# Optimization experiments

Hardware: AMD Instinct MI355X
Metric: run time of the kernel (lower is better)

## Reference

```python
import jax, jax.numpy as jnp
import numpy as np

B, T, D, H = 256, 1024, 64, 128


def _orthogonal(key, shape):
    a = jax.random.normal(key, (max(shape), max(shape)), dtype=jnp.float32)
    q, _ = jnp.linalg.qr(a)
    return q[: shape[0], : shape[1]].astype(jnp.float32)


def setup_inputs() -> dict:
    key = jax.random.key(0)
    k0, k1, k2, k3 = jax.random.split(key, 4)
    x = jax.random.normal(k0, (B, T, D), dtype=jnp.float32)
    W_xK = _orthogonal(k1, (H, D))
    W_xz = _orthogonal(k2, (H, D))
    W_hK = _orthogonal(k3, (H, H))
    b_xK = jnp.zeros((H,), jnp.float32)
    b_xz = jnp.zeros((H,), jnp.float32)
    b_hK = jnp.zeros((H,), jnp.float32)
    return {"x": x, "W_xK": W_xK, "b_xK": b_xK, "W_xz": W_xz,
            "b_xz": b_xz, "W_hK": W_hK, "b_hK": b_hK}


def reference(x, W_xK, b_xK, W_xz, b_xz, W_hK, b_hK):
    # Precompute input projections for all timesteps (batched GEMM).
    gate_x_K = jnp.einsum('btd,hd->bth', x, W_xK) + b_xK  # [B,T,H]
    gate_x_z = jnp.einsum('btd,hd->bth', x, W_xz) + b_xz  # [B,T,H]
    z_all = jnp.tanh(gate_x_z)                             # [B,T,H]
    h0 = jnp.zeros((x.shape[0], W_hK.shape[0]), x.dtype)

    def step(h, inputs):
        gxK, z = inputs  # each [B,H]
        gate_h_K = h @ W_hK.T + b_hK
        K_gain = jax.nn.sigmoid(gxK + gate_h_K)
        h_new = jnp.tanh(h + K_gain * (z - h))
        return h_new, h_new

    # scan over time dim
    _, outs = jax.lax.scan(step, h0,
                           (jnp.swapaxes(gate_x_K, 0, 1),
                            jnp.swapaxes(z_all, 0, 1)))
    outs = jnp.swapaxes(outs, 0, 1)  # [B,T,H]
    return (outs, outs)
```

## Files before the change

### kernel.cpp

```cpp
#include <hip/hip_runtime.h>
#include <hip/hip_fp16.h>

#define NB 256
#define NT 1024
#define ND 64
#define NH 128

typedef __fp16 half8 __attribute__((ext_vector_type(8)));
typedef float float4v __attribute__((ext_vector_type(4)));

static __device__ __forceinline__ float fast_tanh(float v) {
    float e = __expf(2.0f * v);
    return 1.0f - 2.0f * __builtin_amdgcn_rcpf(e + 1.0f);
}

static __device__ __forceinline__ void fast_barrier() {
    asm volatile("s_waitcnt lgkmcnt(0)\n\ts_barrier" ::: "memory");
}

__global__ __launch_bounds__(256, 1) void fused_rnn_mfma(
        const float* __restrict__ x,
        const float* __restrict__ WxK, const float* __restrict__ bxK,
        const float* __restrict__ Wxz, const float* __restrict__ bxz,
        const float* __restrict__ Whk, const float* __restrict__ bhk,
        float* __restrict__ out) {
    __shared__ __align__(16) __fp16 hbuf[2][128];
    __shared__ __align__(16) __fp16 gbuf[2][16][132];
    __shared__ __align__(16) __fp16 zbuf[2][16][132];

    const int tid = threadIdx.x;
    const int b = blockIdx.x;
    const int wid = tid >> 6, lane = tid & 63;
    const int l16 = lane & 15, kg = lane >> 4;
    const int jl = lane & 31;
    const int j = wid * 32 + jl;

    half8 whT[2][4];
    half8 wxT[2][2][2];
    float bGK[2], bZ[2];
    #pragma unroll
    for (int ct = 0; ct < 2; ++ct) {
        const int row = wid * 32 + ct * 16 + l16;
        #pragma unroll
        for (int kt = 0; kt < 4; ++kt) {
            const float* p = Whk + (size_t)row * NH + kt * 32 + kg * 8;
            float4v u = *(const float4v*)p, v = *(const float4v*)(p + 4);
            whT[ct][kt] = (half8){(__fp16)u.x, (__fp16)u.y, (__fp16)u.z, (__fp16)u.w,
                                  (__fp16)v.x, (__fp16)v.y, (__fp16)v.z, (__fp16)v.w};
        }
        #pragma unroll
        for (int mat = 0; mat < 2; ++mat) {
            const float* W = mat ? Wxz : WxK;
            #pragma unroll
            for (int kt = 0; kt < 2; ++kt) {
                const float* p = W + (size_t)row * ND + kt * 32 + kg * 8;
                float4v u = *(const float4v*)p, v = *(const float4v*)(p + 4);
                wxT[mat][ct][kt] = (half8){(__fp16)u.x, (__fp16)u.y, (__fp16)u.z, (__fp16)u.w,
                                           (__fp16)v.x, (__fp16)v.y, (__fp16)v.z, (__fp16)v.w};
            }
        }
        bGK[ct] = bxK[row] + bhk[row];
        bZ[ct]  = bxz[row];
    }
    const float4v zero4 = {0.f, 0.f, 0.f, 0.f};

    const float* xb = x + (size_t)b * NT * ND;
    float4v xf[4];

    auto xload = [&](int c) {
        const float* px = xb + (size_t)c * 16 * 64 + (size_t)l16 * 64;
        #pragma unroll
        for (int kt = 0; kt < 2; ++kt) {
            const float* q = px + kt * 32 + kg * 8;
            xf[2 * kt]     = *(const float4v*)q;
            xf[2 * kt + 1] = *(const float4v*)(q + 4);
        }
    };

    auto proj = [&](int dst) {
        half8 ax[2];
        #pragma unroll
        for (int kt = 0; kt < 2; ++kt) {
            float4v u = xf[2 * kt], v = xf[2 * kt + 1];
            ax[kt] = (half8){(__fp16)u.x, (__fp16)u.y, (__fp16)u.z, (__fp16)u.w,
                             (__fp16)v.x, (__fp16)v.y, (__fp16)v.z, (__fp16)v.w};
        }
        #pragma unroll
        for (int mat = 0; mat < 2; ++mat)
            #pragma unroll
            for (int ct = 0; ct < 2; ++ct) {
                float4v pc = __builtin_amdgcn_mfma_f32_16x16x32_f16(ax[0], wxT[mat][ct][0], zero4, 0, 0, 0);
                pc = __builtin_amdgcn_mfma_f32_16x16x32_f16(ax[1], wxT[mat][ct][1], pc, 0, 0, 0);
                const int col = wid * 32 + ct * 16 + l16;
                #pragma unroll
                for (int r = 0; r < 4; ++r) {
                    const int row = kg * 4 + r;
                    if (mat == 0) gbuf[dst][row][col] = (__fp16)(pc[r] + bGK[ct]);
                    else          zbuf[dst][row][col] = (__fp16)fast_tanh(pc[r] + bZ[ct]);
                }
            }
    };

    xload(0);
    if (tid < 128) hbuf[0][tid] = (__fp16)0.0f;
    proj(0);
    xload(1);
    __syncthreads();

    float hn = 0.0f;
    float oreg[16];
    const size_t CPY = (size_t)NB * NT * NH;
    float* ob = out + (size_t)b * NT * NH + j;

    for (int c = 0; c < 64; ++c) {
        const int cb = c & 1;

        #pragma unroll
        for (int s = 0; s < 16; ++s) {
            const int p = s & 1;
            half8 ah0 = *(const half8*)&hbuf[p][0 * 32 + kg * 8];
            half8 ah1 = *(const half8*)&hbuf[p][1 * 32 + kg * 8];
            half8 ah2 = *(const half8*)&hbuf[p][2 * 32 + kg * 8];
            half8 ah3 = *(const half8*)&hbuf[p][3 * 32 + kg * 8];
            const float gv = (float)gbuf[cb][s][j];
            const float zv = (float)zbuf[cb][s][j];

            float4v aA0 = __builtin_amdgcn_mfma_f32_16x16x32_f16(ah0, whT[0][0], zero4, 0, 0, 0);
            float4v aA1 = __builtin_amdgcn_mfma_f32_16x16x32_f16(ah0, whT[1][0], zero4, 0, 0, 0);
            float4v aB0 = __builtin_amdgcn_mfma_f32_16x16x32_f16(ah2, whT[0][2], zero4, 0, 0, 0);
            float4v aB1 = __builtin_amdgcn_mfma_f32_16x16x32_f16(ah2, whT[1][2], zero4, 0, 0, 0);
            aA0 = __builtin_amdgcn_mfma_f32_16x16x32_f16(ah1, whT[0][1], aA0, 0, 0, 0);
            aA1 = __builtin_amdgcn_mfma_f32_16x16x32_f16(ah1, whT[1][1], aA1, 0, 0, 0);
            aB0 = __builtin_amdgcn_mfma_f32_16x16x32_f16(ah3, whT[0][3], aB0, 0, 0, 0);
            aB1 = __builtin_amdgcn_mfma_f32_16x16x32_f16(ah3, whT[1][3], aB1, 0, 0, 0);

            const bool hi = (jl & 16) != 0;
            const float ya = hi ? aA1[0] : aA0[0];
            const float yb = hi ? aB1[0] : aB0[0];

            const float pre = (ya + yb) + gv;
            const float K = __builtin_amdgcn_rcpf(1.0f + __expf(-pre));
            hn = fast_tanh(__builtin_fmaf(K, zv - hn, hn));
            oreg[s] = hn;

            if (lane < 32) hbuf[p ^ 1][j] = (__fp16)hn;
            fast_barrier();
        }

        if (lane < 32) {
            float* po = ob + (size_t)(c * 16) * NH;
            #pragma unroll
            for (int s = 0; s < 16; ++s) {
                po[(size_t)s * NH] = oreg[s];
                po[CPY + (size_t)s * NH] = oreg[s];
            }
        }

        if (c < 63) {
            proj(cb ^ 1);
            if (c < 62) xload(c + 2);
        }
    }
}

extern "C" void kernel_launch(void* const* d_in, const int* in_sizes, int n_in,
                              void* d_out, int out_size, void* d_ws, size_t ws_size,
                              hipStream_t stream) {
    (void)in_sizes; (void)n_in; (void)d_ws; (void)ws_size; (void)out_size;
    const float* x   = (const float*)d_in[0];
    const float* WxK = (const float*)d_in[1];
    const float* bxK = (const float*)d_in[2];
    const float* Wxz = (const float*)d_in[3];
    const float* bxz = (const float*)d_in[4];
    const float* Whk = (const float*)d_in[5];
    const float* bhk = (const float*)d_in[6];
    float* out = (float*)d_out;

    fused_rnn_mfma<<<256, 256, 0, stream>>>(x, WxK, bxK, Wxz, bxz, Whk, bhk, out);
}
```

Before: 542.1 us.

## Replace recurrent MFMA matvec with packed fp16 dot2 and DPP reductions

The per-step recurrent h@W_hK product is now done with v_dot2 packed-fp16 instructions. Each group of 4 lanes splits the K dimension and combines partial sums with DPP xor reductions, replacing eight MFMA ops whose results were mostly discarded. Each thread now owns two hidden units. Gate and z projections are stored transposed, so each thread loads a whole chunk of 16 timesteps from LDS at once rather than reading one value per step. The two output copies are written by different lanes. The aim is to shorten the serial per-timestep latency chain, at the cost of more VALU work and more registers for the weights.

```diff
diff --git a/kernel.cpp b/kernel.cpp
--- a/kernel.cpp
+++ b/kernel.cpp
@@ -7,6 +7,8 @@
 #define NH 128
 
 typedef __fp16 half8 __attribute__((ext_vector_type(8)));
+typedef __fp16 half4v __attribute__((ext_vector_type(4)));
+typedef __fp16 half2v __attribute__((ext_vector_type(2)));
 typedef float float4v __attribute__((ext_vector_type(4)));
 
 static __device__ __forceinline__ float fast_tanh(float v) {
@@ -14,40 +16,72 @@
     return 1.0f - 2.0f * __builtin_amdgcn_rcpf(e + 1.0f);
 }
 
+static __device__ __forceinline__ float fdot2f(half2v a, half2v b, float c) {
+#if __has_builtin(__builtin_amdgcn_fdot2)
+    return __builtin_amdgcn_fdot2(a, b, c, false);
+#else
+    return c + (float)a.x * (float)b.x + (float)a.y * (float)b.y;
+#endif
+}
+
 static __device__ __forceinline__ void fast_barrier() {
     asm volatile("s_waitcnt lgkmcnt(0)\n\ts_barrier" ::: "memory");
 }
 
-__global__ __launch_bounds__(256, 1) void fused_rnn_mfma(
+static __device__ __forceinline__ float dpp_xor1_add(float x) {
+#if __has_builtin(__builtin_amdgcn_mov_dpp)
+    int o = __builtin_amdgcn_mov_dpp(__builtin_bit_cast(int, x), 0xB1, 0xF, 0xF, true);
+    return x + __builtin_bit_cast(float, o);
+#else
+    return x + __shfl_xor(x, 1);
+#endif
+}
+
+static __device__ __forceinline__ float dpp_xor2_add(float x) {
+#if __has_builtin(__builtin_amdgcn_mov_dpp)
+    int o = __builtin_amdgcn_mov_dpp(__builtin_bit_cast(int, x), 0x4E, 0xF, 0xF, true);
+    return x + __builtin_bit_cast(float, o);
+#else
+    return x + __shfl_xor(x, 2);
+#endif
+}
+
+__global__ __launch_bounds__(256, 1) void fused_rnn_v7(
         const float* __restrict__ x,
         const float* __restrict__ WxK, const float* __restrict__ bxK,
         const float* __restrict__ Wxz, const float* __restrict__ bxz,
         const float* __restrict__ Whk, const float* __restrict__ bhk,
         float* __restrict__ out) {
     __shared__ __align__(16) __fp16 hbuf[2][128];
-    __shared__ __align__(16) __fp16 gbuf[2][16][132];
-    __shared__ __align__(16) __fp16 zbuf[2][16][132];
+    __shared__ __align__(16) __fp16 gT[2][128][24];
+    __shared__ __align__(16) __fp16 zT[2][128][24];
 
     const int tid = threadIdx.x;
     const int b = blockIdx.x;
-    const int wid = tid >> 6, lane = tid & 63;
+    const int w = tid >> 6, lane = tid & 63;
     const int l16 = lane & 15, kg = lane >> 4;
-    const int jl = lane & 31;
-    const int j = wid * 32 + jl;
-
-    half8 whT[2][4];
+    const int q = (tid >> 2) & 15, kh = tid & 3;
+    const int j0 = w * 32 + q, j1 = j0 + 16;
+
+    half2v w0[16], w1[16];
+    {
+        const float4v* p0 = (const float4v*)(Whk + (size_t)j0 * NH + kh * 32);
+        const float4v* p1 = (const float4v*)(Whk + (size_t)j1 * NH + kh * 32);
+        #pragma unroll
+        for (int i = 0; i < 8; ++i) {
+            float4v v0 = p0[i], v1 = p1[i];
+            w0[2 * i]     = __builtin_amdgcn_cvt_pkrtz(v0.x, v0.y);
+            w0[2 * i + 1] = __builtin_amdgcn_cvt_pkrtz(v0.z, v0.w);
+            w1[2 * i]     = __builtin_amdgcn_cvt_pkrtz(v1.x, v1.y);
+            w1[2 * i + 1] = __builtin_amdgcn_cvt_pkrtz(v1.z, v1.w);
+        }
+    }
+
     half8 wxT[2][2][2];
     float bGK[2], bZ[2];
     #pragma unroll
     for (int ct = 0; ct < 2; ++ct) {
-        const int row = wid * 32 + ct * 16 + l16;
-        #pragma unroll
-        for (int kt = 0; kt < 4; ++kt) {
-            const float* p = Whk + (size_t)row * NH + kt * 32 + kg * 8;
-            float4v u = *(const float4v*)p, v = *(const float4v*)(p + 4);
-            whT[ct][kt] = (half8){(__fp16)u.x, (__fp16)u.y, (__fp16)u.z, (__fp16)u.w,
-                                  (__fp16)v.x, (__fp16)v.y, (__fp16)v.z, (__fp16)v.w};
-        }
+        const int row = w * 32 + ct * 16 + l16;
         #pragma unroll
         for (int mat = 0; mat < 2; ++mat) {
             const float* W = mat ? Wxz : WxK;
@@ -71,9 +105,9 @@
         const float* px = xb + (size_t)c * 16 * 64 + (size_t)l16 * 64;
         #pragma unroll
         for (int kt = 0; kt < 2; ++kt) {
-            const float* q = px + kt * 32 + kg * 8;
-            xf[2 * kt]     = *(const float4v*)q;
-            xf[2 * kt + 1] = *(const float4v*)(q + 4);
+            const float* qp = px + kt * 32 + kg * 8;
+            xf[2 * kt]     = *(const float4v*)qp;
+            xf[2 * kt + 1] = *(const float4v*)(qp + 4);
         }
     };
 
@@ -86,19 +120,19 @@
                              (__fp16)v.x, (__fp16)v.y, (__fp16)v.z, (__fp16)v.w};
         }
         #pragma unroll
-        for (int mat = 0; mat < 2; ++mat)
-            #pragma unroll
-            for (int ct = 0; ct < 2; ++ct) {
-                float4v pc = __builtin_amdgcn_mfma_f32_16x16x32_f16(ax[0], wxT[mat][ct][0], zero4, 0, 0, 0);
-                pc = __builtin_amdgcn_mfma_f32_16x16x32_f16(ax[1], wxT[mat][ct][1], pc, 0, 0, 0);
-                const int col = wid * 32 + ct * 16 + l16;
-                #pragma unroll
-                for (int r = 0; r < 4; ++r) {
-                    const int row = kg * 4 + r;
-                    if (mat == 0) gbuf[dst][row][col] = (__fp16)(pc[r] + bGK[ct]);
-                    else          zbuf[dst][row][col] = (__fp16)fast_tanh(pc[r] + bZ[ct]);
-                }
-            }
+        for (int ct = 0; ct < 2; ++ct) {
+            const int col = w * 32 + ct * 16 + l16;
+            float4v pg = __builtin_amdgcn_mfma_f32_16x16x32_f16(ax[0], wxT[0][ct][0], zero4, 0, 0, 0);
+            pg = __builtin_amdgcn_mfma_f32_16x16x32_f16(ax[1], wxT[0][ct][1], pg, 0, 0, 0);
+            half4v hg = {(__fp16)(pg[0] + bGK[ct]), (__fp16)(pg[1] + bGK[ct]),
+                         (__fp16)(pg[2] + bGK[ct]), (__fp16)(pg[3] + bGK[ct])};
+            *(half4v*)&gT[dst][col][kg * 4] = hg;
+            float4v pz = __builtin_amdgcn_mfma_f32_16x16x32_f16(ax[0], wxT[1][ct][0], zero4, 0, 0, 0);
+            pz = __builtin_amdgcn_mfma_f32_16x16x32_f16(ax[1], wxT[1][ct][1], pz, 0, 0, 0);
+            half4v hz = {(__fp16)fast_tanh(pz[0] + bZ[ct]), (__fp16)fast_tanh(pz[1] + bZ[ct]),
+                         (__fp16)fast_tanh(pz[2] + bZ[ct]), (__fp16)fast_tanh(pz[3] + bZ[ct])};
+            *(half4v*)&zT[dst][col][kg * 4] = hz;
+        }
     };
 
     xload(0);
@@ -107,52 +141,76 @@
     xload(1);
     __syncthreads();
 
-    float hn = 0.0f;
-    float oreg[16];
+    float hn0 = 0.0f, hn1 = 0.0f;
+    float oreg0[16], oreg1[16];
     const size_t CPY = (size_t)NB * NT * NH;
-    float* ob = out + (size_t)b * NT * NH + j;
+    float* obase = out + (size_t)b * NT * NH + (kh == 1 ? CPY : 0);
 
     for (int c = 0; c < 64; ++c) {
         const int cb = c & 1;
 
+        half8 g0a = *(const half8*)&gT[cb][j0][0], g0b = *(const half8*)&gT[cb][j0][8];
+        half8 g1a = *(const half8*)&gT[cb][j1][0], g1b = *(const half8*)&gT[cb][j1][8];
+        half8 z0a = *(const half8*)&zT[cb][j0][0], z0b = *(const half8*)&zT[cb][j0][8];
+        half8 z1a = *(const half8*)&zT[cb][j1][0], z1b = *(const half8*)&zT[cb][j1][8];
+
         #pragma unroll
         for (int s = 0; s < 16; ++s) {
             const int p = s & 1;
-            half8 ah0 = *(const half8*)&hbuf[p][0 * 32 + kg * 8];
-            half8 ah1 = *(const half8*)&hbuf[p][1 * 32 + kg * 8];
-            half8 ah2 = *(const half8*)&hbuf[p][2 * 32 + kg * 8];
-            half8 ah3 = *(const half8*)&hbuf[p][3 * 32 + kg * 8];
-            const float gv = (float)gbuf[cb][s][j];
-            const float zv = (float)zbuf[cb][s][j];
-
-            float4v aA0 = __builtin_amdgcn_mfma_f32_16x16x32_f16(ah0, whT[0][0], zero4, 0, 0, 0);
-            float4v aA1 = __builtin_amdgcn_mfma_f32_16x16x32_f16(ah0, whT[1][0], zero4, 0, 0, 0);
-            float4v aB0 = __builtin_amdgcn_mfma_f32_16x16x32_f16(ah2, whT[0][2], zero4, 0, 0, 0);
-            float4v aB1 = __builtin_amdgcn_mfma_f32_16x16x32_f16(ah2, whT[1][2], zero4, 0, 0, 0);
-            aA0 = __builtin_amdgcn_mfma_f32_16x16x32_f16(ah1, whT[0][1], aA0, 0, 0, 0);
-            aA1 = __builtin_amdgcn_mfma_f32_16x16x32_f16(ah1, whT[1][1], aA1, 0, 0, 0);
-            aB0 = __builtin_amdgcn_mfma_f32_16x16x32_f16(ah3, whT[0][3], aB0, 0, 0, 0);
-            aB1 = __builtin_amdgcn_mfma_f32_16x16x32_f16(ah3, whT[1][3], aB1, 0, 0, 0);
-
-            const bool hi = (jl & 16) != 0;
-            const float ya = hi ? aA1[0] : aA0[0];
-            const float yb = hi ? aB1[0] : aB0[0];
-
-            const float pre = (ya + yb) + gv;
-            const float K = __builtin_amdgcn_rcpf(1.0f + __expf(-pre));
-            hn = fast_tanh(__builtin_fmaf(K, zv - hn, hn));
-            oreg[s] = hn;
-
-            if (lane < 32) hbuf[p ^ 1][j] = (__fp16)hn;
+            half8 ah0 = *(const half8*)&hbuf[p][kh * 32 + 0];
+            half8 ah1 = *(const half8*)&hbuf[p][kh * 32 + 8];
+            half8 ah2 = *(const half8*)&hbuf[p][kh * 32 + 16];
+            half8 ah3 = *(const half8*)&hbuf[p][kh * 32 + 24];
+
+            const float gv0 = (float)(s < 8 ? g0a[s & 7] : g0b[s & 7]);
+            const float gv1 = (float)(s < 8 ? g1a[s & 7] : g1b[s & 7]);
+            const float zv0 = (float)(s < 8 ? z0a[s & 7] : z0b[s & 7]);
+            const float zv1 = (float)(s < 8 ? z1a[s & 7] : z1b[s & 7]);
+            const float d0 = zv0 - hn0;
+            const float d1 = zv1 - hn1;
+
+            float a0 = 0.f, a1 = 0.f, a2 = 0.f, a3 = 0.f;
+            float c0 = 0.f, c1 = 0.f, c2 = 0.f, c3 = 0.f;
+            #pragma unroll
+            for (int blk = 0; blk < 4; ++blk) {
+                const half8 hv = blk == 0 ? ah0 : blk == 1 ? ah1 : blk == 2 ? ah2 : ah3;
+                const half2v h01 = __builtin_shufflevector(hv, hv, 0, 1);
+                const half2v h23 = __builtin_shufflevector(hv, hv, 2, 3);
+                const half2v h45 = __builtin_shufflevector(hv, hv, 4, 5);
+                const half2v h67 = __builtin_shufflevector(hv, hv, 6, 7);
+                a0 = fdot2f(w0[4 * blk + 0], h01, a0);
+                a1 = fdot2f(w0[4 * blk + 1], h23, a1);
+                a2 = fdot2f(w0[4 * blk + 2], h45, a2);
+                a3 = fdot2f(w0[4 * blk + 3], h67, a3);
+                c0 = fdot2f(w1[4 * blk + 0], h01, c0);
+                c1 = fdot2f(w1[4 * blk + 1], h23, c1);
+                c2 = fdot2f(w1[4 * blk + 2], h45, c2);
+                c3 = fdot2f(w1[4 * blk + 3], h67, c3);
+            }
+            const float y0 = dpp_xor2_add(dpp_xor1_add((a0 + a1) + (a2 + a3)));
+            const float y1 = dpp_xor2_add(dpp_xor1_add((c0 + c1) + (c2 + c3)));
+
+            const float K0 = __builtin_amdgcn_rcpf(1.0f + __expf(-(y0 + gv0)));
+            const float K1 = __builtin_amdgcn_rcpf(1.0f + __expf(-(y1 + gv1)));
+            hn0 = fast_tanh(__builtin_fmaf(K0, d0, hn0));
+            hn1 = fast_tanh(__builtin_fmaf(K1, d1, hn1));
+
+            if (kh == 0) {
+                hbuf[p ^ 1][j0] = (__fp16)hn0;
+                hbuf[p ^ 1][j1] = (__fp16)hn1;
+            }
+            oreg0[s] = hn0;
+            oreg1[s] = hn1;
             fast_barrier();
         }
 
-        if (lane < 32) {
-            float* po = ob + (size_t)(c * 16) * NH;
+        if (kh < 2) {
+            float* po = obase + (size_t)(c * 16) * NH;
             #pragma unroll
             for (int s = 0; s < 16; ++s) {
-                po[(size_t)s * NH] = oreg[s];
-                po[CPY + (size_t)s * NH] = oreg[s];
+                po[j0] = oreg0[s];
+                po[j1] = oreg1[s];
+                po += NH;
             }
         }
 
@@ -176,5 +234,5 @@
     const float* bhk = (const float*)d_in[6];
     float* out = (float*)d_out;
 
-    fused_rnn_mfma<<<256, 256, 0, stream>>>(x, WxK, bxK, Wxz, bxz, Whk, bhk, out);
-}
+    fused_rnn_v7<<<256, 256, 0, stream>>>(x, WxK, bxK, Wxz, bxz, Whk, bhk, out);
+}
```

Measured after the change: 607.1 us. 12.0% more time.

## Split hidden units over eight waves and transpose gate buffers for register preload

Applied to the files above, without the earlier changes.

Doubles the block to 512 threads so each wave owns 16 hidden columns, halving the MFMA chain per wave in the serial recurrence step. Gate and z projections are stored transposed per column, so each lane loads a whole chunk's 16 values into registers once instead of doing two LDS reads per step. The two output copies are written by different lane groups in parallel. The cost is eight waves joining every per-step barrier instead of four, which may add synchronisation latency.

```diff
diff --git a/kernel.cpp b/kernel.cpp
--- a/kernel.cpp
+++ b/kernel.cpp
@@ -7,6 +7,7 @@
 #define NH 128
 
 typedef __fp16 half8 __attribute__((ext_vector_type(8)));
+typedef __fp16 half4v __attribute__((ext_vector_type(4)));
 typedef float float4v __attribute__((ext_vector_type(4)));
 
 static __device__ __forceinline__ float fast_tanh(float v) {
@@ -18,50 +19,45 @@
     asm volatile("s_waitcnt lgkmcnt(0)\n\ts_barrier" ::: "memory");
 }
 
-__global__ __launch_bounds__(256, 1) void fused_rnn_mfma(
+__global__ __launch_bounds__(512, 1) void fused_rnn_v8(
         const float* __restrict__ x,
         const float* __restrict__ WxK, const float* __restrict__ bxK,
         const float* __restrict__ Wxz, const float* __restrict__ bxz,
         const float* __restrict__ Whk, const float* __restrict__ bhk,
         float* __restrict__ out) {
     __shared__ __align__(16) __fp16 hbuf[2][128];
-    __shared__ __align__(16) __fp16 gbuf[2][16][132];
-    __shared__ __align__(16) __fp16 zbuf[2][16][132];
+    __shared__ __align__(16) __fp16 gT[2][128][24];
+    __shared__ __align__(16) __fp16 zT[2][128][24];
 
     const int tid = threadIdx.x;
     const int b = blockIdx.x;
-    const int wid = tid >> 6, lane = tid & 63;
+    const int w = tid >> 6, lane = tid & 63;
     const int l16 = lane & 15, kg = lane >> 4;
-    const int jl = lane & 31;
-    const int j = wid * 32 + jl;
+    const int j = w * 16 + l16;
 
-    half8 whT[2][4];
-    half8 wxT[2][2][2];
-    float bGK[2], bZ[2];
+    half8 whT[4];
     #pragma unroll
-    for (int ct = 0; ct < 2; ++ct) {
-        const int row = wid * 32 + ct * 16 + l16;
+    for (int kt = 0; kt < 4; ++kt) {
+        const float* p = Whk + (size_t)j * NH + kt * 32 + kg * 8;
+        float4v u = *(const float4v*)p, v = *(const float4v*)(p + 4);
+        whT[kt] = (half8){(__fp16)u.x, (__fp16)u.y, (__fp16)u.z, (__fp16)u.w,
+                          (__fp16)v.x, (__fp16)v.y, (__fp16)v.z, (__fp16)v.w};
+    }
+
+    half8 wxT[2][2];
+    #pragma unroll
+    for (int mat = 0; mat < 2; ++mat) {
+        const float* W = mat ? Wxz : WxK;
         #pragma unroll
-        for (int kt = 0; kt < 4; ++kt) {
-            const float* p = Whk + (size_t)row * NH + kt * 32 + kg * 8;
+        for (int kt = 0; kt < 2; ++kt) {
+            const float* p = W + (size_t)j * ND + kt * 32 + kg * 8;
             float4v u = *(const float4v*)p, v = *(const float4v*)(p + 4);
-            whT[ct][kt] = (half8){(__fp16)u.x, (__fp16)u.y, (__fp16)u.z, (__fp16)u.w,
-                                  (__fp16)v.x, (__fp16)v.y, (__fp16)v.z, (__fp16)v.w};
+            wxT[mat][kt] = (half8){(__fp16)u.x, (__fp16)u.y, (__fp16)u.z, (__fp16)u.w,
+                                   (__fp16)v.x, (__fp16)v.y, (__fp16)v.z, (__fp16)v.w};
         }
-        #pragma unroll
-        for (int mat = 0; mat < 2; ++mat) {
-            const float* W = mat ? Wxz : WxK;
-            #pragma unroll
-            for (int kt = 0; kt < 2; ++kt) {
-                const float* p = W + (size_t)row * ND + kt * 32 + kg * 8;
-                float4v u = *(const float4v*)p, v = *(const float4v*)(p + 4);
-                wxT[mat][ct][kt] = (half8){(__fp16)u.x, (__fp16)u.y, (__fp16)u.z, (__fp16)u.w,
-                                           (__fp16)v.x, (__fp16)v.y, (__fp16)v.z, (__fp16)v.w};
-            }
-        }
-        bGK[ct] = bxK[row] + bhk[row];
-        bZ[ct]  = bxz[row];
     }
+    const float bGK = bxK[j] + bhk[j];
+    const float bZ  = bxz[j];
     const float4v zero4 = {0.f, 0.f, 0.f, 0.f};
 
     const float* xb = x + (size_t)b * NT * ND;
@@ -71,9 +67,9 @@
         const float* px = xb + (size_t)c * 16 * 64 + (size_t)l16 * 64;
         #pragma unroll
         for (int kt = 0; kt < 2; ++kt) {
-            const float* q = px + kt * 32 + kg * 8;
-            xf[2 * kt]     = *(const float4v*)q;
-            xf[2 * kt + 1] = *(const float4v*)(q + 4);
+            const float* qp = px + kt * 32 + kg * 8;
+            xf[2 * kt]     = *(const float4v*)qp;
+            xf[2 * kt + 1] = *(const float4v*)(qp + 4);
         }
     };
 
@@ -85,20 +81,16 @@
             ax[kt] = (half8){(__fp16)u.x, (__fp16)u.y, (__fp16)u.z, (__fp16)u.w,
                              (__fp16)v.x, (__fp16)v.y, (__fp16)v.z, (__fp16)v.w};
         }
-        #pragma unroll
-        for (int mat = 0; mat < 2; ++mat)
-            #pragma unroll
-            for (int ct = 0; ct < 2; ++ct) {
-                float4v pc = __builtin_amdgcn_mfma_f32_16x16x32_f16(ax[0], wxT[mat][ct][0], zero4, 0, 0, 0);
-                pc = __builtin_amdgcn_mfma_f32_16x16x32_f16(ax[1], wxT[mat][ct][1], pc, 0, 0, 0);
-                const int col = wid * 32 + ct * 16 + l16;
-                #pragma unroll
-                for (int r = 0; r < 4; ++r) {
-                    const int row = kg * 4 + r;
-                    if (mat == 0) gbuf[dst][row][col] = (__fp16)(pc[r] + bGK[ct]);
-                    else          zbuf[dst][row][col] = (__fp16)fast_tanh(pc[r] + bZ[ct]);
-                }
-            }
+        float4v pg = __builtin_amdgcn_mfma_f32_16x16x32_f16(ax[0], wxT[0][0], zero4, 0, 0, 0);
+        pg = __builtin_amdgcn_mfma_f32_16x16x32_f16(ax[1], wxT[0][1], pg, 0, 0, 0);
+        half4v hg = {(__fp16)(pg[0] + bGK), (__fp16)(pg[1] + bGK),
+                     (__fp16)(pg[2] + bGK), (__fp16)(pg[3] + bGK)};
+        *(half4v*)&gT[dst][j][kg * 4] = hg;
+        float4v pz = __builtin_amdgcn_mfma_f32_16x16x32_f16(ax[0], wxT[1][0], zero4, 0, 0, 0);
+        pz = __builtin_amdgcn_mfma_f32_16x16x32_f16(ax[1], wxT[1][1], pz, 0, 0, 0);
+        half4v hz = {(__fp16)fast_tanh(pz[0] + bZ), (__fp16)fast_tanh(pz[1] + bZ),
+                     (__fp16)fast_tanh(pz[2] + bZ), (__fp16)fast_tanh(pz[3] + bZ)};
+        *(half4v*)&zT[dst][j][kg * 4] = hz;
     };
 
     xload(0);
@@ -110,10 +102,15 @@
     float hn = 0.0f;
     float oreg[16];
     const size_t CPY = (size_t)NB * NT * NH;
-    float* ob = out + (size_t)b * NT * NH + j;
+    float* obase = out + (size_t)b * NT * NH + (kg == 1 ? CPY : 0);
 
     for (int c = 0; c < 64; ++c) {
         const int cb = c & 1;
+
+        half8 gA = *(const half8*)&gT[cb][j][0];
+        half8 gB = *(const half8*)&gT[cb][j][8];
+        half8 zA = *(const half8*)&zT[cb][j][0];
+        half8 zB = *(const half8*)&zT[cb][j][8];
 
         #pragma unroll
         for (int s = 0; s < 16; ++s) {
@@ -122,37 +119,31 @@
             half8 ah1 = *(const half8*)&hbuf[p][1 * 32 + kg * 8];
             half8 ah2 = *(const half8*)&hbuf[p][2 * 32 + kg * 8];
             half8 ah3 = *(const half8*)&hbuf[p][3 * 32 + kg * 8];
-            const float gv = (float)gbuf[cb][s][j];
-            const float zv = (float)zbuf[cb][s][j];
 
-            float4v aA0 = __builtin_amdgcn_mfma_f32_16x16x32_f16(ah0, whT[0][0], zero4, 0, 0, 0);
-            float4v aA1 = __builtin_amdgcn_mfma_f32_16x16x32_f16(ah0, whT[1][0], zero4, 0, 0, 0);
-            float4v aB0 = __builtin_amdgcn_mfma_f32_16x16x32_f16(ah2, whT[0][2], zero4, 0, 0, 0);
-            float4v aB1 = __builtin_amdgcn_mfma_f32_16x16x32_f16(ah2, whT[1][2], zero4, 0, 0, 0);
-            aA0 = __builtin_amdgcn_mfma_f32_16x16x32_f16(ah1, whT[0][1], aA0, 0, 0, 0);
-            aA1 = __builtin_amdgcn_mfma_f32_16x16x32_f16(ah1, whT[1][1], aA1, 0, 0, 0);
-            aB0 = __builtin_amdgcn_mfma_f32_16x16x32_f16(ah3, whT[0][3], aB0, 0, 0, 0);
-            aB1 = __builtin_amdgcn_mfma_f32_16x16x32_f16(ah3, whT[1][3], aB1, 0, 0, 0);
+            const float gv = (float)(s < 8 ? gA[s & 7] : gB[s & 7]);
+            const float zv = (float)(s < 8 ? zA[s & 7] : zB[s & 7]);
+            const float d = zv - hn;
 
-            const bool hi = (jl & 16) != 0;
-            const float ya = hi ? aA1[0] : aA0[0];
-            const float yb = hi ? aB1[0] : aB0[0];
+            float4v aA = __builtin_amdgcn_mfma_f32_16x16x32_f16(ah0, whT[0], zero4, 0, 0, 0);
+            float4v aB = __builtin_amdgcn_mfma_f32_16x16x32_f16(ah2, whT[2], zero4, 0, 0, 0);
+            aA = __builtin_amdgcn_mfma_f32_16x16x32_f16(ah1, whT[1], aA, 0, 0, 0);
+            aB = __builtin_amdgcn_mfma_f32_16x16x32_f16(ah3, whT[3], aB, 0, 0, 0);
+            const float y = aA[0] + aB[0];
 
-            const float pre = (ya + yb) + gv;
-            const float K = __builtin_amdgcn_rcpf(1.0f + __expf(-pre));
-            hn = fast_tanh(__builtin_fmaf(K, zv - hn, hn));
+            const float K = __builtin_amdgcn_rcpf(1.0f + __expf(-(y + gv)));
+            hn = fast_tanh(__builtin_fmaf(K, d, hn));
             oreg[s] = hn;
 
-            if (lane < 32) hbuf[p ^ 1][j] = (__fp16)hn;
+            if (kg == 0) hbuf[p ^ 1][j] = (__fp16)hn;
             fast_barrier();
         }
 
-        if (lane < 32) {
-            float* po = ob + (size_t)(c * 16) * NH;
+        if (kg < 2) {
+            float* po = obase + (size_t)(c * 16) * NH;
             #pragma unroll
             for (int s = 0; s < 16; ++s) {
-                po[(size_t)s * NH] = oreg[s];
-                po[CPY + (size_t)s * NH] = oreg[s];
+                po[j] = oreg[s];
+                po += NH;
             }
         }
 
@@ -176,5 +167,5 @@
     const float* bhk = (const float*)d_in[6];
     float* out = (float*)d_out;
 
-    fused_rnn_mfma<<<256, 256, 0, stream>>>(x, WxK, bxK, Wxz, bxz, Whk, bhk, out);
+    fused_rnn_v8<<<256, 512, 0, stream>>>(x, WxK, bxK, Wxz, bxz, Whk, bhk, out);
 }
```

Result: faster. 502.5 us (-7.3%).
